# Performance work log

Measured on AMD Instinct MI355X. Metric: run time of the kernel, lower is better.

## Reference

```python
import jax, jax.numpy as jnp
import numpy as np

K = 10  # hardcoded in the module
F = 3 + 3 * K + 3 * K + K + 3  # 76-dim per-point feature


def setup_inputs() -> dict:
    key = jax.random.key(0)
    k0, k1, k2, k3, k4 = jax.random.split(key, 5)
    B, N = 4, 8192
    input_cloud = jax.random.normal(k0, (B, N, 3), dtype=jnp.float32)
    # Single shared MLP (76 -> 64 -> 3); the original instantiates a fresh
    # randomly-initialized MLP per point, which a fused kernel replaces with
    # shared weights.
    W1 = jax.random.normal(k1, (F, 64), dtype=jnp.float32) * 0.1
    b1 = jax.random.normal(k2, (64,), dtype=jnp.float32) * 0.01
    W2 = jax.random.normal(k3, (64, 3), dtype=jnp.float32) * 0.1
    b2 = jax.random.normal(k4, (3,), dtype=jnp.float32) * 0.01
    return {"input_cloud": input_cloud, "W1": W1, "b1": b1, "W2": W2, "b2": b2}


def _knn_indices(cloud):
    # squared pairwise distances (same ordering as cdist), topk smallest
    sq = jnp.sum(cloud * cloud, axis=-1)  # [B,N]
    d2 = sq[:, :, None] + sq[:, None, :] - 2.0 * jnp.einsum("bnd,bmd->bnm", cloud, cloud)
    _, idx = jax.lax.top_k(-d2, K + 1)  # [B,N,K+1], smallest first (self at 0)
    return idx[:, :, 1:]  # drop self -> [B,N,K]


def reference(input_cloud, W1, b1, W2, b2):
    B, N, _ = input_cloud.shape
    knn_idx = _knn_indices(input_cloud)  # [B,N,K] int32

    # gather neighbors: [B,N,K,3]
    neighbors = jnp.take_along_axis(input_cloud[:, None, :, :],
                                    knn_idx[:, :, :, None], axis=2)
    center = input_cloud  # [B,N,3]
    rel = neighbors - center[:, :, None, :]           # [B,N,K,3]
    dists = jnp.sqrt(jnp.sum(rel * rel, axis=-1))     # [B,N,K]

    # per-point 3x3 covariance of the K neighbors (unbiased, like torch.cov)
    mean = jnp.mean(neighbors, axis=2, keepdims=True)  # [B,N,1,3]
    cen = neighbors - mean
    cov = jnp.einsum("bnki,bnkj->bnij", cen, cen) / (K - 1)  # [B,N,3,3]

    eig = jnp.linalg.eigvalsh(cov)          # ascending [B,N,3]
    l1, l2, l3 = eig[..., 2], eig[..., 1], eig[..., 0]  # descending order
    linearity = (l1 - l2) / l1
    planarity = (l2 - l3) / l1
    scattering = l3 / l1
    geom = jnp.stack([linearity, planarity, scattering], axis=-1)  # [B,N,3]

    feats = jnp.concatenate(
        [center,
         neighbors.reshape(B, N, 3 * K),
         rel.reshape(B, N, 3 * K),
         dists,
         geom], axis=-1)  # [B,N,76]

    h = jax.nn.relu(jnp.einsum("bnf,fh->bnh", feats, W1) + b1)
    out = jax.nn.relu(jnp.einsum("bnh,ho->bno", h, W2) + b2)  # [B,N,3]
    return out
```

## Files before the change

### kernel.cpp

```cpp
#include <hip/hip_runtime.h>
#include <math.h>

#define KNN    10
#define NPTS   8192
#define HID    64
#define NF     76
#define Q      16
#define CAP    64
#define F32_INF __uint_as_float(0x7F800000u)

typedef float v2f __attribute__((ext_vector_type(2)));

__device__ __forceinline__ float rl(float v, int lane) {
    return __int_as_float(__builtin_amdgcn_readlane(__float_as_int(v), lane));
}

__global__ __launch_bounds__(256) void soa_kernel(const float* __restrict__ cloud,
                                                  float* __restrict__ soa) {
    const int i = blockIdx.x * 256 + threadIdx.x;
    const float x = cloud[i * 3 + 0];
    const float y = cloud[i * 3 + 1];
    const float z = cloud[i * 3 + 2];
    soa[i]             = x;
    soa[4 * NPTS + i]  = y;
    soa[8 * NPTS + i]  = z;
}

__global__ __launch_bounds__(256) void knn_kernel(const float* __restrict__ soa,
                                                  unsigned short* __restrict__ knn_idx) {
    __shared__ unsigned long long coll[CAP][Q + 1];
    __shared__ float pk[4][Q][17];
    __shared__ float tau_s[Q];
    __shared__ int   cnt[Q];

    const int t    = threadIdx.x;
    const int w    = t >> 6;
    const int lane = t & 63;
    const int h    = w;
    const int bx   = blockIdx.x;
    const int b    = bx >> 9;
    const int n_base = (bx & 511) * Q;
    const int cb0 = h * (NPTS / 4);

    const float* __restrict__ xs = soa + (size_t)b * NPTS;
    const float* __restrict__ ys = xs + 4 * NPTS;
    const float* __restrict__ zs = xs + 8 * NPTS;

    if (t < Q) cnt[t] = 0;

    v2f qx_p[8], qy_p[8], qz_p[8];
    {
        const int ql = n_base + (lane & 15);
        const float lx = xs[ql];
        const float ly = ys[ql];
        const float lz = zs[ql];
#pragma unroll
        for (int j = 0; j < 8; ++j) {
            qx_p[j] = (v2f){ rl(lx, 2 * j), rl(lx, 2 * j + 1) };
            qy_p[j] = (v2f){ rl(ly, 2 * j), rl(ly, 2 * j + 1) };
            qz_p[j] = (v2f){ rl(lz, 2 * j), rl(lz, 2 * j + 1) };
        }
    }

#define LOADT(TI, RX, RY, RZ) do {                        \
        const int c_ = cb0 + (((TI) & 31) * 64) + lane;   \
        (RX) = xs[c_]; (RY) = ys[c_]; (RZ) = zs[c_];      \
    } while (0)

#define P1_BODY(CX, CY, CZ) do {                                          \
        const float aw_ = fmaf((CZ), (CZ), fmaf((CY), (CY), (CX)*(CX)));  \
        const v2f aw2_ = (v2f){ aw_, aw_ };                               \
        const v2f ax2_ = (v2f){ -2.0f * (CX), -2.0f * (CX) };             \
        const v2f ay2_ = (v2f){ -2.0f * (CY), -2.0f * (CY) };             \
        const v2f az2_ = (v2f){ -2.0f * (CZ), -2.0f * (CZ) };             \
        _Pragma("unroll")                                                 \
        for (int j_ = 0; j_ < 8; ++j_) {                                  \
            const v2f v_ = __builtin_elementwise_fma(ax2_, qx_p[j_],      \
                           __builtin_elementwise_fma(ay2_, qy_p[j_],      \
                           __builtin_elementwise_fma(az2_, qz_p[j_], aw2_))); \
            vmin2[j_] = __builtin_elementwise_min(vmin2[j_], v_);         \
        }                                                                 \
    } while (0)

    v2f vmin2[8];
#pragma unroll
    for (int j = 0; j < 8; ++j) vmin2[j] = (v2f){ F32_INF, F32_INF };

    {
        float x0, y0, z0, x1, y1, z1, x2, y2, z2, x3, y3, z3;
        LOADT(0, x0, y0, z0);
        LOADT(1, x1, y1, z1);
        for (int k = 0; k < 32; k += 4) {
            LOADT(k + 2, x2, y2, z2);
            LOADT(k + 3, x3, y3, z3);
            P1_BODY(x0, y0, z0);
            P1_BODY(x1, y1, z1);
            LOADT(k + 4, x0, y0, z0);
            LOADT(k + 5, x1, y1, z1);
            P1_BODY(x2, y2, z2);
            P1_BODY(x3, y3, z3);
        }
    }

#pragma unroll
    for (int qq = 0; qq < Q; ++qq) {
        float v = vmin2[qq >> 1][qq & 1];
        v = fminf(v, __shfl_xor(v, 32, 64));
        v = fminf(v, __shfl_xor(v, 16, 64));
        if (lane < 16) pk[w][qq][lane] = v;
    }
    __syncthreads();

    if (w == 0) {
        float md[KNN + 1];
#pragma unroll
        for (int s = 0; s <= KNN; ++s) md[s] = F32_INF;
        const int qsel = lane & 15;
#pragma unroll
        for (int cc = 0; cc < 64; ++cc) {
            float d = pk[cc >> 4][qsel][cc & 15];
#pragma unroll
            for (int u = 0; u <= KNN; ++u) {
                const float lo = fminf(md[u], d);
                d = fmaxf(md[u], d);
                md[u] = lo;
            }
        }
        if (lane < 16) tau_s[lane] = md[KNN] + 1e-3f;
    }
    __syncthreads();

    float taum[Q];
    {
        const float tv = tau_s[lane & 15];
#pragma unroll
        for (int qq = 0; qq < Q; ++qq) taum[qq] = rl(tv, qq);
    }

#define P2_BODY(CX, CY, CZ, TI) do {                                      \
        const int jj_ = cb0 + (TI) * 64 + lane;                           \
        const float aw_ = fmaf((CZ), (CZ), fmaf((CY), (CY), (CX)*(CX)));  \
        const v2f aw2_ = (v2f){ aw_, aw_ };                               \
        const v2f ax2_ = (v2f){ -2.0f * (CX), -2.0f * (CX) };             \
        const v2f ay2_ = (v2f){ -2.0f * (CY), -2.0f * (CY) };             \
        const v2f az2_ = (v2f){ -2.0f * (CZ), -2.0f * (CZ) };             \
        _Pragma("unroll")                                                 \
        for (int j_ = 0; j_ < 8; ++j_) {                                  \
            const v2f v_ = __builtin_elementwise_fma(ax2_, qx_p[j_],      \
                           __builtin_elementwise_fma(ay2_, qy_p[j_],      \
                           __builtin_elementwise_fma(az2_, qz_p[j_], aw2_))); \
            _Pragma("unroll")                                             \
            for (int half_ = 0; half_ < 2; ++half_) {                     \
                const int qq_ = 2 * j_ + half_;                           \
                if (__builtin_expect(v_[half_] <= taum[qq_], 0)) {        \
                    const float qx_ = qx_p[j_][half_];                    \
                    const float qy_ = qy_p[j_][half_];                    \
                    const float qz_ = qz_p[j_][half_];                    \
                    const float qs_ = fmaf(qz_, qz_, fmaf(qy_, qy_, qx_ * qx_)); \
                    const float dot_ = fmaf((CZ), qz_, fmaf((CY), qy_, (CX) * qx_)); \
                    const float d2_ = fmaf(-2.0f, dot_, qs_ + aw_);       \
                    const unsigned int fb_ = __float_as_uint(d2_);        \
                    const unsigned int m_ =                               \
                        fb_ ^ ((unsigned int)((int)fb_ >> 31) | 0x80000000u); \
                    const unsigned long long key_ =                       \
                        ((unsigned long long)m_ << 13) | (unsigned long long)(unsigned)jj_; \
                    const int slot_ = atomicAdd(&cnt[qq_], 1);            \
                    if (slot_ < CAP) coll[slot_][qq_] = key_;             \
                }                                                         \
            }                                                             \
        }                                                                 \
    } while (0)

    {
        float x0, y0, z0, x1, y1, z1, x2, y2, z2, x3, y3, z3;
        LOADT(0, x0, y0, z0);
        LOADT(1, x1, y1, z1);
        for (int k = 0; k < 32; k += 4) {
            LOADT(k + 2, x2, y2, z2);
            LOADT(k + 3, x3, y3, z3);
            P2_BODY(x0, y0, z0, k + 0);
            P2_BODY(x1, y1, z1, k + 1);
            LOADT(k + 4, x0, y0, z0);
            LOADT(k + 5, x1, y1, z1);
            P2_BODY(x2, y2, z2, k + 2);
            P2_BODY(x3, y3, z3, k + 3);
        }
    }
    __syncthreads();

    if (t < Q) {
        const int m = cnt[t];
        int mc = m;
#pragma unroll
        for (int off = 1; off < 16; off <<= 1)
            mc = max(mc, __shfl_xor(mc, off, 64));
        mc = __builtin_amdgcn_readfirstlane(mc);

        const int n = (bx & 511) * Q + t;

        unsigned long long md[KNN + 1];
#pragma unroll
        for (int s = 0; s <= KNN; ++s) md[s] = ~0ULL;

        if (mc <= CAP) {
            for (int cc = 0; cc < mc; ++cc) {
                unsigned long long key = (cc < m) ? coll[cc][t] : ~0ULL;
#pragma unroll
                for (int u = 0; u <= KNN; ++u) {
                    const bool lt = key < md[u];
                    const unsigned long long lo = lt ? key : md[u];
                    key = lt ? md[u] : key;
                    md[u] = lo;
                }
            }
        } else {
            const float qx = xs[n];
            const float qy = ys[n];
            const float qz = zs[n];
            const float qs = fmaf(qz, qz, fmaf(qy, qy, qx * qx));
            for (int j = 0; j < NPTS; ++j) {
                const float px = xs[j];
                const float py = ys[j];
                const float pz = zs[j];
                const float pw = fmaf(pz, pz, fmaf(py, py, px * px));
                const float dot = fmaf(pz, qz, fmaf(py, qy, px * qx));
                const float d2 = fmaf(-2.0f, dot, qs + pw);
                const unsigned int fb = __float_as_uint(d2);
                const unsigned int mm =
                    fb ^ ((unsigned int)((int)fb >> 31) | 0x80000000u);
                unsigned long long key =
                    ((unsigned long long)mm << 13) | (unsigned long long)j;
                key = (j == n) ? ~0ULL : key;
#pragma unroll
                for (int u = 0; u <= KNN; ++u) {
                    const bool lt = key < md[u];
                    const unsigned long long lo = lt ? key : md[u];
                    key = lt ? md[u] : key;
                    md[u] = lo;
                }
            }
        }

        unsigned short* outp = knn_idx + ((size_t)b * NPTS + n) * KNN;
        int outc = 0;
#pragma unroll
        for (int u = 0; u <= KNN; ++u) {
            const int idx = (int)(md[u] & 8191u);
            if (outc < KNN && idx != n) outp[outc++] = (unsigned short)idx;
        }
    }
#undef LOADT
#undef P1_BODY
#undef P2_BODY
}

__global__ __launch_bounds__(256) void feat_mlp_kernel(const float* __restrict__ cloud,
                                                       const float* __restrict__ W1,
                                                       const float* __restrict__ b1,
                                                       const float* __restrict__ W2,
                                                       const float* __restrict__ b2,
                                                       const unsigned short* __restrict__ knn_idx,
                                                       float* __restrict__ out) {
    __shared__ float w1s[NF * 68];
    __shared__ float b1s[HID];
    __shared__ float w2s[HID * 3];
    __shared__ float b2s[3];
    __shared__ float fs[64][NF + 1];

    const int t = threadIdx.x;
    for (int idx = t; idx < NF * HID; idx += 256)
        w1s[(idx >> 6) * 68 + (idx & 63)] = W1[idx];
    if (t < HID) b1s[t] = b1[t];
    if (t < HID * 3) w2s[t] = W2[t];
    if (t < 3) b2s[t] = b2[t];

    const int pl   = t >> 2;
    const int s    = t & 3;
    const int subh = t & 1;
    const int subf = (t >> 1) & 1;
    const int gid = blockIdx.x * 64 + pl;
    const int b = gid >> 13;
    const int n = gid & (NPTS - 1);
    const float* cb = cloud + (size_t)b * NPTS * 3;

    {
        const float cx = cb[n * 3 + 0];
        const float cy = cb[n * 3 + 1];
        const float cz = cb[n * 3 + 2];

        const int kbase = (s == 0) ? 0 : (s == 1) ? 3 : (s == 2) ? 6 : 8;
        const int kcnt  = (s < 2) ? 3 : 2;

        float nx[3], ny[3], nz[3];
        const unsigned short* ki = knn_idx + (size_t)gid * KNN;
        for (int kk = 0; kk < kcnt; ++kk) {
            const int j = ki[kbase + kk];
            nx[kk] = cb[j * 3 + 0];
            ny[kk] = cb[j * 3 + 1];
            nz[kk] = cb[j * 3 + 2];
        }

        float* fr = fs[pl];
        if (s == 0) { fr[0] = cx; fr[1] = cy; fr[2] = cz; }
        for (int kk = 0; kk < kcnt; ++kk) {
            const int k = kbase + kk;
            fr[3 + 3 * k + 0] = nx[kk];
            fr[3 + 3 * k + 1] = ny[kk];
            fr[3 + 3 * k + 2] = nz[kk];
            const float rx = nx[kk] - cx, ry = ny[kk] - cy, rz = nz[kk] - cz;
            fr[33 + 3 * k + 0] = rx;
            fr[33 + 3 * k + 1] = ry;
            fr[33 + 3 * k + 2] = rz;
            fr[63 + k] = sqrtf(fmaf(rz, rz, fmaf(ry, ry, rx * rx)));
        }

        float smx = 0.f, smy = 0.f, smz = 0.f;
        for (int kk = 0; kk < kcnt; ++kk) { smx += nx[kk]; smy += ny[kk]; smz += nz[kk]; }
#define QSUM(v) { v += __shfl_xor(v, 1, 64); v += __shfl_xor(v, 2, 64); }
        QSUM(smx); QSUM(smy); QSUM(smz);
        const float mx = smx * (1.0f / KNN);
        const float my = smy * (1.0f / KNN);
        const float mz = smz * (1.0f / KNN);

        float c00 = 0.f, c01 = 0.f, c02 = 0.f, c11 = 0.f, c12 = 0.f, c22 = 0.f;
        for (int kk = 0; kk < kcnt; ++kk) {
            const float ex = nx[kk] - mx, ey = ny[kk] - my, ez = nz[kk] - mz;
            c00 = fmaf(ex, ex, c00); c01 = fmaf(ex, ey, c01); c02 = fmaf(ex, ez, c02);
            c11 = fmaf(ey, ey, c11); c12 = fmaf(ey, ez, c12); c22 = fmaf(ez, ez, c22);
        }
        QSUM(c00); QSUM(c01); QSUM(c02); QSUM(c11); QSUM(c12); QSUM(c22);
#undef QSUM
        const float sc = 1.0f / (KNN - 1);
        c00 *= sc; c01 *= sc; c02 *= sc; c11 *= sc; c12 *= sc; c22 *= sc;

        const float qd = (c00 + c11 + c22) * (1.0f / 3.0f);
        const float pp1 = c01 * c01 + c02 * c02 + c12 * c12;
        const float d00 = c00 - qd, d11 = c11 - qd, d22 = c22 - qd;
        const float p2 = d00 * d00 + d11 * d11 + d22 * d22 + 2.0f * pp1;
        float l1, l2, l3;
        if (p2 < 1e-30f) {
            l1 = l2 = l3 = qd;
        } else {
            const float p = sqrtf(p2 * (1.0f / 6.0f));
            const float inv = 1.0f / p;
            const float e00 = d00 * inv, e11 = d11 * inv, e22 = d22 * inv;
            const float e01 = c01 * inv, e02 = c02 * inv, e12 = c12 * inv;
            float detB = e00 * (e11 * e22 - e12 * e12)
                       - e01 * (e01 * e22 - e12 * e02)
                       + e02 * (e01 * e12 - e11 * e02);
            float r = 0.5f * detB;
            r = fminf(1.0f, fmaxf(-1.0f, r));
            const float phi = acosf(r) * (1.0f / 3.0f);
            l1 = qd + 2.0f * p * __cosf(phi);
            l3 = qd + 2.0f * p * __cosf(phi + 2.0943951023931953f);
            l2 = 3.0f * qd - l1 - l3;
        }
        if (s == 0) {
            fr[73] = (l1 - l2) / l1;
            fr[74] = (l2 - l3) / l1;
            fr[75] = l3 / l1;
        }
    }

    __syncthreads();

    const float* fr = fs[pl];
    const int f0 = subf * 38;

    float h[32];
#pragma unroll
    for (int j = 0; j < 32; ++j) h[j] = (subf == 0) ? b1s[subh * 32 + j] : 0.0f;

#pragma unroll 2
    for (int ff = 0; ff < 38; ++ff) {
        const int f = f0 + ff;
        const float v = fr[f];
        const float4* w4 = reinterpret_cast<const float4*>(w1s + f * 68 + subh * 32);
#pragma unroll
        for (int j4 = 0; j4 < 8; ++j4) {
            const float4 w = w4[j4];
            h[4 * j4 + 0] = fmaf(v, w.x, h[4 * j4 + 0]);
            h[4 * j4 + 1] = fmaf(v, w.y, h[4 * j4 + 1]);
            h[4 * j4 + 2] = fmaf(v, w.z, h[4 * j4 + 2]);
            h[4 * j4 + 3] = fmaf(v, w.w, h[4 * j4 + 3]);
        }
    }

#pragma unroll
    for (int j = 0; j < 32; ++j) h[j] += __shfl_xor(h[j], 2, 64);

    float o0 = 0.f, o1 = 0.f, o2 = 0.f;
#pragma unroll
    for (int j = 0; j < 32; ++j) {
        const float r = fmaxf(h[j], 0.0f);
        const int jj = subh * 32 + j;
        o0 = fmaf(r, w2s[jj * 3 + 0], o0);
        o1 = fmaf(r, w2s[jj * 3 + 1], o1);
        o2 = fmaf(r, w2s[jj * 3 + 2], o2);
    }
    o0 += __shfl_xor(o0, 1, 64);
    o1 += __shfl_xor(o1, 1, 64);
    o2 += __shfl_xor(o2, 1, 64);

    if ((t & 3) == 0) {
        float* op = out + (size_t)gid * 3;
        op[0] = fmaxf(o0 + b2s[0], 0.0f);
        op[1] = fmaxf(o1 + b2s[1], 0.0f);
        op[2] = fmaxf(o2 + b2s[2], 0.0f);
    }
}

extern "C" void kernel_launch(void* const* d_in, const int* in_sizes, int n_in,
                              void* d_out, int out_size, void* d_ws, size_t ws_size,
                              hipStream_t stream) {
    const float* cloud = (const float*)d_in[0];
    const float* W1    = (const float*)d_in[1];
    const float* b1    = (const float*)d_in[2];
    const float* W2    = (const float*)d_in[3];
    const float* b2    = (const float*)d_in[4];
    float* out = (float*)d_out;

    unsigned short* knn = (unsigned short*)d_ws;
    float* soa = (float*)((char*)d_ws + 655360);

    soa_kernel<<<dim3(128), dim3(256), 0, stream>>>(cloud, soa);
    knn_kernel<<<dim3(2048), dim3(256), 0, stream>>>(soa, knn);
    feat_mlp_kernel<<<dim3(512), dim3(256), 0, stream>>>(cloud, W1, b1, W2, b2, knn, out);
}
```

Before: 171.2 us.

## Split fused KNN kernel into threshold pass and collection pass kernels

```diff
diff --git a/kernel.cpp b/kernel.cpp
--- a/kernel.cpp
+++ b/kernel.cpp
@@ -26,27 +26,21 @@
     soa[8 * NPTS + i]  = z;
 }
 
-__global__ __launch_bounds__(256) void knn_kernel(const float* __restrict__ soa,
-                                                  unsigned short* __restrict__ knn_idx) {
-    __shared__ unsigned long long coll[CAP][Q + 1];
+__global__ __launch_bounds__(256) void knn_pass1(const float* __restrict__ soa,
+                                                 float* __restrict__ tau_g) {
     __shared__ float pk[4][Q][17];
-    __shared__ float tau_s[Q];
-    __shared__ int   cnt[Q];
 
     const int t    = threadIdx.x;
     const int w    = t >> 6;
     const int lane = t & 63;
-    const int h    = w;
     const int bx   = blockIdx.x;
     const int b    = bx >> 9;
     const int n_base = (bx & 511) * Q;
-    const int cb0 = h * (NPTS / 4);
+    const int cb0 = w * (NPTS / 4);
 
     const float* __restrict__ xs = soa + (size_t)b * NPTS;
     const float* __restrict__ ys = xs + 4 * NPTS;
     const float* __restrict__ zs = xs + 8 * NPTS;
-
-    if (t < Q) cnt[t] = 0;
 
     v2f qx_p[8], qy_p[8], qz_p[8];
     {
@@ -126,16 +120,58 @@
                 md[u] = lo;
             }
         }
-        if (lane < 16) tau_s[lane] = md[KNN] + 1e-3f;
+        if (lane < 16) tau_g[bx * Q + lane] = md[KNN] + 1e-3f;
+    }
+#undef LOADT
+#undef P1_BODY
+}
+
+__global__ __launch_bounds__(256) void knn_pass2(const float* __restrict__ soa,
+                                                 const float* __restrict__ tau_g,
+                                                 unsigned short* __restrict__ knn_idx) {
+    __shared__ unsigned long long coll[CAP][Q + 1];
+    __shared__ int cnt[Q];
+
+    const int t    = threadIdx.x;
+    const int w    = t >> 6;
+    const int lane = t & 63;
+    const int bx   = blockIdx.x;
+    const int b    = bx >> 9;
+    const int n_base = (bx & 511) * Q;
+    const int cb0 = w * (NPTS / 4);
+
+    const float* __restrict__ xs = soa + (size_t)b * NPTS;
+    const float* __restrict__ ys = xs + 4 * NPTS;
+    const float* __restrict__ zs = xs + 8 * NPTS;
+
+    if (t < Q) cnt[t] = 0;
+
+    v2f qx_p[8], qy_p[8], qz_p[8];
+    {
+        const int ql = n_base + (lane & 15);
+        const float lx = xs[ql];
+        const float ly = ys[ql];
+        const float lz = zs[ql];
+#pragma unroll
+        for (int j = 0; j < 8; ++j) {
+            qx_p[j] = (v2f){ rl(lx, 2 * j), rl(lx, 2 * j + 1) };
+            qy_p[j] = (v2f){ rl(ly, 2 * j), rl(ly, 2 * j + 1) };
+            qz_p[j] = (v2f){ rl(lz, 2 * j), rl(lz, 2 * j + 1) };
+        }
+    }
+
+    float taum[Q];
+    {
+        const float tv = tau_g[bx * Q + (lane & 15)];
+#pragma unroll
+        for (int qq = 0; qq < Q; ++qq) taum[qq] = rl(tv, qq);
     }
     __syncthreads();
 
-    float taum[Q];
-    {
-        const float tv = tau_s[lane & 15];
-#pragma unroll
-        for (int qq = 0; qq < Q; ++qq) taum[qq] = rl(tv, qq);
-    }
+#define LOADT(TI, RX, RY, RZ) do {                        \
+        const int c_ = cb0 + (((TI) & 31) * 64) + lane;   \
+        (RX) = xs[c_]; (RY) = ys[c_]; (RZ) = zs[c_];      \
+    } while (0)
 
 #define P2_BODY(CX, CY, CZ, TI) do {                                      \
         const int jj_ = cb0 + (TI) * 64 + lane;                           \
@@ -250,7 +286,6 @@
         }
     }
 #undef LOADT
-#undef P1_BODY
 #undef P2_BODY
 }
 
@@ -421,9 +456,11 @@
     float* out = (float*)d_out;
 
     unsigned short* knn = (unsigned short*)d_ws;
-    float* soa = (float*)((char*)d_ws + 655360);
+    float* soa   = (float*)((char*)d_ws + 655360);
+    float* tau_g = (float*)((char*)d_ws + 655360 + 393216);
 
     soa_kernel<<<dim3(128), dim3(256), 0, stream>>>(cloud, soa);
-    knn_kernel<<<dim3(2048), dim3(256), 0, stream>>>(soa, knn);
+    knn_pass1<<<dim3(2048), dim3(256), 0, stream>>>(soa, tau_g);
+    knn_pass2<<<dim3(2048), dim3(256), 0, stream>>>(soa, tau_g, knn);
     feat_mlp_kernel<<<dim3(512), dim3(256), 0, stream>>>(cloud, W1, b1, W2, b2, knn, out);
 }
```

Result: faster. 166.4 us (median of 3 runs) (-2.8%).

## Fuse feature extraction and MLP into the KNN kernel tail

Applied to the files above, without the earlier changes.

```diff
diff --git a/kernel.cpp b/kernel.cpp
--- a/kernel.cpp
+++ b/kernel.cpp
@@ -26,21 +26,27 @@
     soa[8 * NPTS + i]  = z;
 }
 
-__global__ __launch_bounds__(256) void knn_kernel(const float* __restrict__ soa,
-                                                  unsigned short* __restrict__ knn_idx) {
+__global__ __launch_bounds__(256) void knn_feat_kernel(const float* __restrict__ soa,
+                                                       const float* __restrict__ cloud,
+                                                       const float* __restrict__ W1,
+                                                       const float* __restrict__ b1,
+                                                       const float* __restrict__ W2,
+                                                       const float* __restrict__ b2,
+                                                       float* __restrict__ out) {
     __shared__ unsigned long long coll[CAP][Q + 1];
     __shared__ float pk[4][Q][17];
     __shared__ float tau_s[Q];
     __shared__ int   cnt[Q];
+    __shared__ unsigned short nbr[Q][KNN];
+    __shared__ float fs[Q][NF + 1];
 
     const int t    = threadIdx.x;
     const int w    = t >> 6;
     const int lane = t & 63;
-    const int h    = w;
     const int bx   = blockIdx.x;
     const int b    = bx >> 9;
     const int n_base = (bx & 511) * Q;
-    const int cb0 = h * (NPTS / 4);
+    const int cb0 = w * (NPTS / 4);
 
     const float* __restrict__ xs = soa + (size_t)b * NPTS;
     const float* __restrict__ ys = xs + 4 * NPTS;
@@ -196,7 +202,7 @@
             mc = max(mc, __shfl_xor(mc, off, 64));
         mc = __builtin_amdgcn_readfirstlane(mc);
 
-        const int n = (bx & 511) * Q + t;
+        const int n = n_base + t;
 
         unsigned long long md[KNN + 1];
 #pragma unroll
@@ -241,49 +247,21 @@
             }
         }
 
-        unsigned short* outp = knn_idx + ((size_t)b * NPTS + n) * KNN;
         int outc = 0;
 #pragma unroll
         for (int u = 0; u <= KNN; ++u) {
             const int idx = (int)(md[u] & 8191u);
-            if (outc < KNN && idx != n) outp[outc++] = (unsigned short)idx;
-        }
-    }
-#undef LOADT
-#undef P1_BODY
-#undef P2_BODY
-}
-
-__global__ __launch_bounds__(256) void feat_mlp_kernel(const float* __restrict__ cloud,
-                                                       const float* __restrict__ W1,
-                                                       const float* __restrict__ b1,
-                                                       const float* __restrict__ W2,
-                                                       const float* __restrict__ b2,
-                                                       const unsigned short* __restrict__ knn_idx,
-                                                       float* __restrict__ out) {
-    __shared__ float w1s[NF * 68];
-    __shared__ float b1s[HID];
-    __shared__ float w2s[HID * 3];
-    __shared__ float b2s[3];
-    __shared__ float fs[64][NF + 1];
-
-    const int t = threadIdx.x;
-    for (int idx = t; idx < NF * HID; idx += 256)
-        w1s[(idx >> 6) * 68 + (idx & 63)] = W1[idx];
-    if (t < HID) b1s[t] = b1[t];
-    if (t < HID * 3) w2s[t] = W2[t];
-    if (t < 3) b2s[t] = b2[t];
-
-    const int pl   = t >> 2;
-    const int s    = t & 3;
-    const int subh = t & 1;
-    const int subf = (t >> 1) & 1;
-    const int gid = blockIdx.x * 64 + pl;
-    const int b = gid >> 13;
-    const int n = gid & (NPTS - 1);
-    const float* cb = cloud + (size_t)b * NPTS * 3;
-
-    {
+            if (outc < KNN && idx != n) nbr[t][outc++] = (unsigned short)idx;
+        }
+    }
+    __syncthreads();
+
+    if (w == 0) {
+        const int pl   = t >> 2;
+        const int s    = t & 3;
+        const int n    = n_base + pl;
+        const float* cb = cloud + (size_t)b * NPTS * 3;
+
         const float cx = cb[n * 3 + 0];
         const float cy = cb[n * 3 + 1];
         const float cz = cb[n * 3 + 2];
@@ -292,9 +270,8 @@
         const int kcnt  = (s < 2) ? 3 : 2;
 
         float nx[3], ny[3], nz[3];
-        const unsigned short* ki = knn_idx + (size_t)gid * KNN;
         for (int kk = 0; kk < kcnt; ++kk) {
-            const int j = ki[kbase + kk];
+            const int j = nbr[pl][kbase + kk];
             nx[kk] = cb[j * 3 + 0];
             ny[kk] = cb[j * 3 + 1];
             nz[kk] = cb[j * 3 + 2];
@@ -361,53 +338,61 @@
             fr[75] = l3 / l1;
         }
     }
-
     __syncthreads();
 
-    const float* fr = fs[pl];
-    const int f0 = subf * 38;
-
-    float h[32];
-#pragma unroll
-    for (int j = 0; j < 32; ++j) h[j] = (subf == 0) ? b1s[subh * 32 + j] : 0.0f;
+    if (w == 0) {
+        const int pl   = t >> 2;
+        const int subh = t & 1;
+        const int subf = (t >> 1) & 1;
+        const float* fr = fs[pl];
+        const int f0 = subf * 38;
+
+        float h[32];
+#pragma unroll
+        for (int j = 0; j < 32; ++j) h[j] = (subf == 0) ? b1[subh * 32 + j] : 0.0f;
 
 #pragma unroll 2
-    for (int ff = 0; ff < 38; ++ff) {
-        const int f = f0 + ff;
-        const float v = fr[f];
-        const float4* w4 = reinterpret_cast<const float4*>(w1s + f * 68 + subh * 32);
-#pragma unroll
-        for (int j4 = 0; j4 < 8; ++j4) {
-            const float4 w = w4[j4];
-            h[4 * j4 + 0] = fmaf(v, w.x, h[4 * j4 + 0]);
-            h[4 * j4 + 1] = fmaf(v, w.y, h[4 * j4 + 1]);
-            h[4 * j4 + 2] = fmaf(v, w.z, h[4 * j4 + 2]);
-            h[4 * j4 + 3] = fmaf(v, w.w, h[4 * j4 + 3]);
-        }
-    }
-
-#pragma unroll
-    for (int j = 0; j < 32; ++j) h[j] += __shfl_xor(h[j], 2, 64);
-
-    float o0 = 0.f, o1 = 0.f, o2 = 0.f;
-#pragma unroll
-    for (int j = 0; j < 32; ++j) {
-        const float r = fmaxf(h[j], 0.0f);
-        const int jj = subh * 32 + j;
-        o0 = fmaf(r, w2s[jj * 3 + 0], o0);
-        o1 = fmaf(r, w2s[jj * 3 + 1], o1);
-        o2 = fmaf(r, w2s[jj * 3 + 2], o2);
-    }
-    o0 += __shfl_xor(o0, 1, 64);
-    o1 += __shfl_xor(o1, 1, 64);
-    o2 += __shfl_xor(o2, 1, 64);
-
-    if ((t & 3) == 0) {
-        float* op = out + (size_t)gid * 3;
-        op[0] = fmaxf(o0 + b2s[0], 0.0f);
-        op[1] = fmaxf(o1 + b2s[1], 0.0f);
-        op[2] = fmaxf(o2 + b2s[2], 0.0f);
-    }
+        for (int ff = 0; ff < 38; ++ff) {
+            const int f = f0 + ff;
+            const float v = fr[f];
+            const float4* w4 = reinterpret_cast<const float4*>(W1 + f * 64 + subh * 32);
+#pragma unroll
+            for (int j4 = 0; j4 < 8; ++j4) {
+                const float4 wv = w4[j4];
+                h[4 * j4 + 0] = fmaf(v, wv.x, h[4 * j4 + 0]);
+                h[4 * j4 + 1] = fmaf(v, wv.y, h[4 * j4 + 1]);
+                h[4 * j4 + 2] = fmaf(v, wv.z, h[4 * j4 + 2]);
+                h[4 * j4 + 3] = fmaf(v, wv.w, h[4 * j4 + 3]);
+            }
+        }
+
+#pragma unroll
+        for (int j = 0; j < 32; ++j) h[j] += __shfl_xor(h[j], 2, 64);
+
+        float o0 = 0.f, o1 = 0.f, o2 = 0.f;
+#pragma unroll
+        for (int j = 0; j < 32; ++j) {
+            const float r = fmaxf(h[j], 0.0f);
+            const int jj = subh * 32 + j;
+            o0 = fmaf(r, W2[jj * 3 + 0], o0);
+            o1 = fmaf(r, W2[jj * 3 + 1], o1);
+            o2 = fmaf(r, W2[jj * 3 + 2], o2);
+        }
+        o0 += __shfl_xor(o0, 1, 64);
+        o1 += __shfl_xor(o1, 1, 64);
+        o2 += __shfl_xor(o2, 1, 64);
+
+        if ((t & 3) == 0) {
+            const int n = n_base + pl;
+            float* op = out + ((size_t)b * NPTS + n) * 3;
+            op[0] = fmaxf(o0 + b2[0], 0.0f);
+            op[1] = fmaxf(o1 + b2[1], 0.0f);
+            op[2] = fmaxf(o2 + b2[2], 0.0f);
+        }
+    }
+#undef LOADT
+#undef P1_BODY
+#undef P2_BODY
 }
 
 extern "C" void kernel_launch(void* const* d_in, const int* in_sizes, int n_in,
@@ -420,10 +405,8 @@
     const float* b2    = (const float*)d_in[4];
     float* out = (float*)d_out;
 
-    unsigned short* knn = (unsigned short*)d_ws;
-    float* soa = (float*)((char*)d_ws + 655360);
+    float* soa = (float*)d_ws;
 
     soa_kernel<<<dim3(128), dim3(256), 0, stream>>>(cloud, soa);
-    knn_kernel<<<dim3(2048), dim3(256), 0, stream>>>(soa, knn);
-    feat_mlp_kernel<<<dim3(512), dim3(256), 0, stream>>>(cloud, W1, b1, W2, b2, knn, out);
+    knn_feat_kernel<<<dim3(2048), dim3(256), 0, stream>>>(soa, cloud, W1, b1, W2, b2, out);
 }
```

New measurement: 192.9 us. 1.13x slower.
